# Performance work log

Hardware: AMD Instinct MI355X
Metric: run time of the kernel (lower is better)

## Reference

```python
import jax, jax.numpy as jnp
import numpy as np

L = 16384   # nodes (rows)
E = 131072  # edges
SP = 20000  # column positions (nodes + periodic images)
C = 512     # embed_dim
H = 8       # heads
DH = C // H # head dim = 64
HID = 1024  # ffn hidden


def setup_inputs() -> dict:
    key = jax.random.key(0)
    ks = jax.random.split(key, 16)
    p = lambda k, shape: jax.random.normal(k, shape, dtype=jnp.float32) * 0.02
    return dict(
        x=jax.random.normal(ks[0], (L, C), dtype=jnp.float32),
        row_index=jax.random.randint(ks[1], (E,), 0, L),
        col_index=jax.random.randint(ks[2], (E,), 0, L),
        to_col_index=jax.random.randint(ks[3], (E,), 0, SP),
        att_bias=jax.random.normal(ks[4], (E, H), dtype=jnp.float32),
        pos_att_bias=jax.random.normal(ks[5], (E, H), dtype=jnp.float32),
        dist=jax.random.uniform(ks[6], (E,), minval=0.5, maxval=5.0),
        pos=jax.random.normal(ks[7], (L, 3), dtype=jnp.float32),
        col_pos=jax.random.normal(ks[8], (SP, 3), dtype=jnp.float32),
        ln1_g=jnp.ones((C,), jnp.float32), ln1_b=jnp.zeros((C,), jnp.float32),
        ln2_g=jnp.ones((C,), jnp.float32), ln2_b=jnp.zeros((C,), jnp.float32),
        Wq=p(ks[9], (C, C)), bq=jnp.zeros((C,), jnp.float32),
        Wk=p(ks[10], (C, C)), bk=jnp.zeros((C,), jnp.float32),
        Wv=p(ks[11], (C, C)), bv=jnp.zeros((C,), jnp.float32),
        Wvec=p(ks[12], (3, C)), bvec=jnp.zeros((C,), jnp.float32),
        Wo=p(ks[13], (C, C)), bo=jnp.zeros((C,), jnp.float32),
        W1=p(ks[14], (C, HID)), b1=jnp.zeros((HID,), jnp.float32),
        W2=p(ks[15], (HID, C)), b2=jnp.zeros((C,), jnp.float32),
    )


def _ln(x, g, b, eps=1e-5):
    mu = jnp.mean(x, -1, keepdims=True)
    v = jnp.mean((x - mu) ** 2, -1, keepdims=True)
    return (x - mu) * jax.lax.rsqrt(v + eps) * g + b


def reference(x, row_index, col_index, to_col_index, att_bias, pos_att_bias,
              dist, pos, col_pos, ln1_g, ln1_b, ln2_g, ln2_b,
              Wq, bq, Wk, bk, Wv, bv, Wvec, bvec, Wo, bo, W1, b1, W2, b2):
    Lx = x.shape[0]
    # --- pre-norm + Euclidean sparse attention ---
    z = _ln(x, ln1_g, ln1_b)
    q = (z @ Wq + bq).reshape(Lx, H, DH)
    k = (z @ Wk + bk).reshape(Lx, H, DH)
    v = (z @ Wv + bv).reshape(Lx, H, DH)
    qe = q[row_index]          # (E,H,DH) gather
    ke = k[col_index]          # (E,H,DH)
    ve = v[col_index]          # (E,H,DH)
    # relative unit direction from receiving node to (PBC-shifted) column node
    rel = (col_pos[to_col_index] - pos[row_index]) / dist[:, None]   # (E,3)
    ve = ve + (rel @ Wvec + bvec).reshape(-1, H, DH)
    # Euclidean (negative squared L2) attention score + positional bias
    score = -jnp.sum((qe - ke) ** 2, axis=-1) / np.float32(np.sqrt(DH)) + pos_att_bias  # (E,H)
    # segment softmax over edges grouped by row_index
    m = jax.ops.segment_max(score, row_index, num_segments=Lx)       # (L,H)
    m = jnp.where(jnp.isfinite(m), m, 0.0)
    pexp = jnp.exp(score - m[row_index])
    den = jax.ops.segment_sum(pexp, row_index, num_segments=Lx)      # (L,H)
    deng = den[row_index]
    alpha = pexp / jnp.where(deng == 0.0, 1.0, deng)                 # (E,H)
    out = jax.ops.segment_sum(alpha[:, :, None] * ve, row_index, num_segments=Lx)
    att = out.reshape(Lx, C) @ Wo + bo
    x = x + att
    # --- pre-norm + feed-forward ---
    z2 = _ln(x, ln2_g, ln2_b)
    ff = jax.nn.gelu(z2 @ W1 + b1) @ W2 + b2
    return x + ff
```

## Files before the change

kernel.cpp:

```cpp
#include <hip/hip_runtime.h>

#define L_NODES 16384
#define E_EDGES 131072
#define CDIM 512
#define QKVDIM 1536
#define HEADS 8
#define DHEAD 64
#define HID 1024

typedef __attribute__((ext_vector_type(8))) short bf16x8;
typedef __attribute__((ext_vector_type(4))) float f32x4;

__device__ inline unsigned short f2b(float f) {
    union { float f; unsigned int u; } v{f};
    unsigned int r = (v.u + 0x7fffu + ((v.u >> 16) & 1u)) >> 16;
    return (unsigned short)r;
}
__device__ inline float b2f(unsigned short h) {
    union { unsigned int u; float f; } v;
    v.u = (unsigned int)h << 16;
    return v.f;
}

__device__ inline void async_lds16(const void* g, void* l) {
    __builtin_amdgcn_global_load_lds(
        (const __attribute__((address_space(1))) unsigned int*)g,
        (__attribute__((address_space(3))) unsigned int*)l,
        16, 0, 0);
}

__global__ __launch_bounds__(256) void ln_bf16_kernel(
    const float* __restrict__ x, const float* __restrict__ g,
    const float* __restrict__ b, short* __restrict__ out)
{
    int row = blockIdx.x;
    int t = threadIdx.x;
    const float2* xr = (const float2*)(x + (size_t)row * CDIM);
    float2 v = xr[t];
    float s = v.x + v.y;
    float sq = v.x * v.x + v.y * v.y;
    for (int off = 32; off; off >>= 1) {
        s += __shfl_xor(s, off);
        sq += __shfl_xor(sq, off);
    }
    __shared__ float ss[4], sqs[4];
    int wave = t >> 6, lane = t & 63;
    if (lane == 0) { ss[wave] = s; sqs[wave] = sq; }
    __syncthreads();
    s = ss[0] + ss[1] + ss[2] + ss[3];
    sq = sqs[0] + sqs[1] + sqs[2] + sqs[3];
    float mu = s * (1.0f / CDIM);
    float var = sq * (1.0f / CDIM) - mu * mu;
    float inv = rsqrtf(var + 1e-5f);
    int c = t * 2;
    unsigned short h0 = f2b((v.x - mu) * inv * g[c] + b[c]);
    unsigned short h1 = f2b((v.y - mu) * inv * g[c + 1] + b[c + 1]);
    unsigned int packed = ((unsigned int)h1 << 16) | h0;
    *(unsigned int*)(out + (size_t)row * CDIM + c) = packed;
}

__global__ __launch_bounds__(256) void prep_kernel(
    const float* __restrict__ Wq, const float* __restrict__ Wk,
    const float* __restrict__ Wv, const float* __restrict__ Wo,
    const float* __restrict__ W1, const float* __restrict__ W2,
    short* __restrict__ wqkvT, short* __restrict__ woT,
    short* __restrict__ w1T, short* __restrict__ w2T,
    const float* __restrict__ bq, const float* __restrict__ bk,
    const float* __restrict__ bv, float* __restrict__ bqkv,
    int* __restrict__ cnt)
{
    int bid = blockIdx.x;
    if (bid >= 2054) {
        cnt[(bid - 2054) * 256 + threadIdx.x] = 0;
        return;
    }
    if (bid >= 2048) {
        int i = (bid - 2048) * 256 + threadIdx.x;
        float val = (i < CDIM) ? bq[i] : (i < 2 * CDIM) ? bk[i - CDIM] : bv[i - 2 * CDIM];
        bqkv[i] = val;
        return;
    }
    const float* W; short* WT; int K, N, tn, tk;
    if (bid < 1024) {
        int w = bid >> 8, local = bid & 255;
        tn = local & 15; tk = local >> 4; K = 512; N = 512;
        W = (w == 0) ? Wq : (w == 1) ? Wk : (w == 2) ? Wv : Wo;
        WT = (w == 3) ? woT : wqkvT + (size_t)w * 512 * 512;
    } else if (bid < 1536) {
        int local = bid - 1024;
        tn = local & 31; tk = local >> 5; K = 512; N = 1024;
        W = W1; WT = w1T;
    } else {
        int local = bid - 1536;
        tn = local & 15; tk = local >> 4; K = 1024; N = 512;
        W = W2; WT = w2T;
    }
    __shared__ float tile[32][33];
    int tx = threadIdx.x & 31, ty = threadIdx.x >> 5;
    int n0 = tn * 32, k0 = tk * 32;
#pragma unroll
    for (int r = 0; r < 4; r++)
        tile[ty + r * 8][tx] = W[(size_t)(k0 + ty + r * 8) * N + n0 + tx];
    __syncthreads();
#pragma unroll
    for (int r = 0; r < 4; r++)
        WT[(size_t)(n0 + ty + r * 8) * K + k0 + tx] = f2b(tile[tx][ty + r * 8]);
}

template<int BM>
__global__ __launch_bounds__(256) void gemm_bf16_kernel(
    const short* __restrict__ A, const short* __restrict__ B,
    const float* __restrict__ bias, const float* __restrict__ res,
    float* __restrict__ outf, short* __restrict__ outb,
    int M, int N, int K, int act)
{
    constexpr int MI = BM / 32;
    constexpr int LPI_A = BM / 64;
    constexpr int STAGE_A = BM * 64;
    constexpr int STAGE_B = 8192;
    __shared__ short As[3 * BM * 32];
    __shared__ short Bs[3 * 128 * 32];
    int t = threadIdx.x;
    int bm = blockIdx.y * BM, bn = blockIdx.x * 128;
    int wave = t >> 6, lane = t & 63;
    int wm = (wave & 1) * (BM / 2), wn = (wave >> 1) * 64;
    int crow = lane & 15, quad = lane >> 4;

    f32x4 acc[MI][4] = {};

    const int niter = K >> 5;
    auto stage = [&](int s, int k0) {
#pragma unroll
        for (int a = 0; a < LPI_A; a++) {
            int idx = a * 256 + t;
            int row = idx >> 2, chunk = idx & 3;
            async_lds16(A + (size_t)(bm + row) * K + k0 + chunk * 8,
                        (char*)As + s * STAGE_A + idx * 16);
        }
#pragma unroll
        for (int c = 0; c < 2; c++) {
            int idx = c * 256 + t;
            int row = idx >> 2, chunk = idx & 3;
            async_lds16(B + (size_t)(bn + row) * K + k0 + chunk * 8,
                        (char*)Bs + s * STAGE_B + idx * 16);
        }
    };

    stage(0, 0);
    stage(1, 32);

    for (int i = 0; i < niter; ++i) {
        int cur = i % 3;
        if (i + 1 < niter) {
            if constexpr (BM == 256)      asm volatile("s_waitcnt vmcnt(6)" ::: "memory");
            else if constexpr (BM == 128) asm volatile("s_waitcnt vmcnt(4)" ::: "memory");
            else                          asm volatile("s_waitcnt vmcnt(3)" ::: "memory");
        } else {
            asm volatile("s_waitcnt vmcnt(0)" ::: "memory");
        }
        __builtin_amdgcn_s_barrier();
        if (i + 2 < niter) stage((i + 2) % 3, (i + 2) << 5);

        const short* Ab = As + cur * (BM * 32);
        const short* Bb = Bs + cur * (128 * 32);
        bf16x8 af[MI], bg[4];
#pragma unroll
        for (int ii = 0; ii < MI; ii++)
            af[ii] = *(const bf16x8*)&Ab[(wm + ii * 16 + crow) * 32 + quad * 8];
#pragma unroll
        for (int j = 0; j < 4; j++)
            bg[j] = *(const bf16x8*)&Bb[(wn + j * 16 + crow) * 32 + quad * 8];
#pragma unroll
        for (int ii = 0; ii < MI; ii++)
#pragma unroll
            for (int j = 0; j < 4; j++)
                acc[ii][j] = __builtin_amdgcn_mfma_f32_16x16x32_bf16(af[ii], bg[j], acc[ii][j], 0, 0, 0);
    }

#pragma unroll
    for (int i = 0; i < MI; i++) {
#pragma unroll
        for (int j = 0; j < 4; j++) {
            int n = bn + wn + j * 16 + crow;
            float bi = bias ? bias[n] : 0.0f;
#pragma unroll
            for (int r = 0; r < 4; r++) {
                int mrow = bm + wm + i * 16 + quad * 4 + r;
                float val = acc[i][j][r] + bi;
                if (act) {
                    float u = 1.5957691216057308f * (val + 0.044715f * val * val * val);
                    val = val / (1.0f + __expf(-u));
                }
                if (res) val += res[(size_t)mrow * N + n];
                if (outf) outf[(size_t)mrow * N + n] = val;
                if (outb) outb[(size_t)mrow * N + n] = f2b(val);
            }
        }
    }
}

__global__ void hist_kernel(const int* __restrict__ row_index, int* __restrict__ cnt)
{
    int e = blockIdx.x * 256 + threadIdx.x;
    if (e < E_EDGES) atomicAdd(&cnt[row_index[e]], 1);
}

__global__ __launch_bounds__(1024) void scan_kernel(
    const int* __restrict__ cnt, int* __restrict__ row_start,
    int* __restrict__ cursor)
{
    int t = threadIdx.x;
    int4 c0 = ((const int4*)cnt)[t * 4 + 0];
    int4 c1 = ((const int4*)cnt)[t * 4 + 1];
    int4 c2 = ((const int4*)cnt)[t * 4 + 2];
    int4 c3 = ((const int4*)cnt)[t * 4 + 3];
    int v[16] = {c0.x, c0.y, c0.z, c0.w, c1.x, c1.y, c1.z, c1.w,
                 c2.x, c2.y, c2.z, c2.w, c3.x, c3.y, c3.z, c3.w};
    int total = 0;
    int pfx[16];
#pragma unroll
    for (int i = 0; i < 16; i++) { pfx[i] = total; total += v[i]; }
    int lane = t & 63, wv = t >> 6;
    int incl = total;
    for (int off = 1; off < 64; off <<= 1) {
        int u = __shfl_up(incl, off);
        if (lane >= off) incl += u;
    }
    __shared__ int wsum[16];
    if (lane == 63) wsum[wv] = incl;
    __syncthreads();
    __shared__ int wbase[16];
    if (t < 16) {
        int s = wsum[t];
        int run = 0;
        for (int i = 0; i < 16; i++) { if (i < t) run += wsum[i]; }
        wbase[t] = run;
        (void)s;
    }
    __syncthreads();
    int base = wbase[wv] + (incl - total);
#pragma unroll
    for (int i = 0; i < 4; i++) {
        int4 rs = make_int4(base + pfx[i * 4], base + pfx[i * 4 + 1],
                            base + pfx[i * 4 + 2], base + pfx[i * 4 + 3]);
        ((int4*)row_start)[t * 4 + i] = rs;
        ((int4*)cursor)[t * 4 + i] = rs;
    }
    if (t == 1023) row_start[L_NODES] = base + total;
}

__global__ void scatter_kernel(const int* __restrict__ row_index, const int* __restrict__ col_index,
                               const int* __restrict__ to_col_index, const float* __restrict__ dist,
                               const float* __restrict__ pos, const float* __restrict__ col_pos,
                               const float* __restrict__ pos_att_bias,
                               int* __restrict__ cursor, int4* __restrict__ emeta,
                               float* __restrict__ pabp)
{
    int e = blockIdx.x * 256 + threadIdx.x;
    if (e < E_EDGES) {
        int row = row_index[e];
        int p = atomicAdd(&cursor[row], 1);
        int tci = to_col_index[e];
        float dinv = 1.0f / dist[e];
        float r0 = (col_pos[tci * 3]     - pos[row * 3])     * dinv;
        float r1 = (col_pos[tci * 3 + 1] - pos[row * 3 + 1]) * dinv;
        float r2 = (col_pos[tci * 3 + 2] - pos[row * 3 + 2]) * dinv;
        emeta[p] = make_int4(col_index[e], __float_as_int(r0), __float_as_int(r1),
                             __float_as_int(r2));
        const float4* pb = (const float4*)(pos_att_bias + (size_t)e * HEADS);
        float4 b0 = pb[0], b1 = pb[1];
        float4* dst = (float4*)(pabp + (size_t)p * HEADS);
        dst[0] = b0; dst[1] = b1;
    }
}

__global__ __launch_bounds__(256) void attn_kernel(
    const short* __restrict__ qkv, const int4* __restrict__ emeta,
    const float* __restrict__ pabp, const int* __restrict__ row_start,
    const float* __restrict__ Wvec, const float* __restrict__ bvec,
    short* __restrict__ out_bf)
{
    int lane = threadIdx.x & 63;
    int r = blockIdx.x * 4 + (threadIdx.x >> 6);
    int h = lane >> 3;
    int cbase = lane * 8;

    float qv[8], wv0[8], wv1[8], wv2[8], bvv[8];
    {
        bf16x8 qh = *(const bf16x8*)(qkv + (size_t)r * QKVDIM + cbase);
#pragma unroll
        for (int j = 0; j < 8; j++) qv[j] = b2f((unsigned short)qh[j]);
        float4 a0 = *(const float4*)(Wvec + cbase);
        float4 a1 = *(const float4*)(Wvec + cbase + 4);
        float4 b0 = *(const float4*)(Wvec + CDIM + cbase);
        float4 b1 = *(const float4*)(Wvec + CDIM + cbase + 4);
        float4 c0 = *(const float4*)(Wvec + 2 * CDIM + cbase);
        float4 c1 = *(const float4*)(Wvec + 2 * CDIM + cbase + 4);
        float4 d0 = *(const float4*)(bvec + cbase);
        float4 d1 = *(const float4*)(bvec + cbase + 4);
        wv0[0]=a0.x; wv0[1]=a0.y; wv0[2]=a0.z; wv0[3]=a0.w; wv0[4]=a1.x; wv0[5]=a1.y; wv0[6]=a1.z; wv0[7]=a1.w;
        wv1[0]=b0.x; wv1[1]=b0.y; wv1[2]=b0.z; wv1[3]=b0.w; wv1[4]=b1.x; wv1[5]=b1.y; wv1[6]=b1.z; wv1[7]=b1.w;
        wv2[0]=c0.x; wv2[1]=c0.y; wv2[2]=c0.z; wv2[3]=c0.w; wv2[4]=c1.x; wv2[5]=c1.y; wv2[6]=c1.z; wv2[7]=c1.w;
        bvv[0]=d0.x; bvv[1]=d0.y; bvv[2]=d0.z; bvv[3]=d0.w; bvv[4]=d1.x; bvv[5]=d1.y; bvv[6]=d1.z; bvv[7]=d1.w;
    }

    int e0 = row_start[r], e1 = row_start[r + 1];
    float m = -1e30f, l = 0.0f;
    float acc[8] = {};

    int4 em_n, em_n2;
    float pab_n;
    bf16x8 k_n, v_n;
    if (e0 < e1) {
        em_n = emeta[e0];
        em_n2 = emeta[(e0 + 1 < e1) ? e0 + 1 : e1 - 1];
        pab_n = pabp[(size_t)e0 * HEADS + h];
        const short* kp = qkv + (size_t)em_n.x * QKVDIM + CDIM + cbase;
        k_n = *(const bf16x8*)kp;
        v_n = *(const bf16x8*)(kp + CDIM);
    }
    for (int idx = e0; idx < e1; ++idx) {
        int4 em = em_n;
        float pab = pab_n;
        bf16x8 k8 = k_n, v8 = v_n;
        em_n = em_n2;
        int i2 = (idx + 2 < e1) ? idx + 2 : e1 - 1;
        em_n2 = emeta[i2];
        int i1 = (idx + 1 < e1) ? idx + 1 : e1 - 1;
        pab_n = pabp[(size_t)i1 * HEADS + h];
        {
            const short* kp = qkv + (size_t)em_n.x * QKVDIM + CDIM + cbase;
            k_n = *(const bf16x8*)kp;
            v_n = *(const bf16x8*)(kp + CDIM);
        }
        float s = 0.0f;
        float vf[8];
#pragma unroll
        for (int j = 0; j < 8; j++) {
            float kf = b2f((unsigned short)k8[j]);
            vf[j] = b2f((unsigned short)v8[j]);
            float d = qv[j] - kf;
            s = fmaf(d, d, s);
        }
        s += __shfl_xor(s, 1);
        s += __shfl_xor(s, 2);
        s += __shfl_xor(s, 4);
        float score = -s * 0.125f + pab;
        float mn = fmaxf(m, score);
        float scale = __expf(m - mn);
        float pexp = __expf(score - mn);
        m = mn;
        l = l * scale + pexp;
        float r0 = __int_as_float(em.y), r1 = __int_as_float(em.z), r2 = __int_as_float(em.w);
#pragma unroll
        for (int j = 0; j < 8; j++) {
            float vv = vf[j] + r0 * wv0[j] + r1 * wv1[j] + r2 * wv2[j] + bvv[j];
            acc[j] = fmaf(acc[j], scale, pexp * vv);
        }
    }
    float inv = (l > 0.0f) ? 1.0f / l : 0.0f;
    bf16x8 o;
#pragma unroll
    for (int j = 0; j < 8; j++) o[j] = (short)f2b(acc[j] * inv);
    *(bf16x8*)(out_bf + (size_t)r * CDIM + cbase) = o;
}

extern "C" void kernel_launch(void* const* d_in, const int* in_sizes, int n_in,
                              void* d_out, int out_size, void* d_ws, size_t ws_size,
                              hipStream_t stream)
{
    const float* x            = (const float*)d_in[0];
    const int*   row_index    = (const int*)d_in[1];
    const int*   col_index    = (const int*)d_in[2];
    const int*   to_col_index = (const int*)d_in[3];
    const float* pos_att_bias = (const float*)d_in[5];
    const float* dist         = (const float*)d_in[6];
    const float* pos          = (const float*)d_in[7];
    const float* col_pos      = (const float*)d_in[8];
    const float* ln1_g = (const float*)d_in[9];
    const float* ln1_b = (const float*)d_in[10];
    const float* ln2_g = (const float*)d_in[11];
    const float* ln2_b = (const float*)d_in[12];
    const float* Wq = (const float*)d_in[13];  const float* bq = (const float*)d_in[14];
    const float* Wk = (const float*)d_in[15];  const float* bk = (const float*)d_in[16];
    const float* Wv = (const float*)d_in[17];  const float* bv = (const float*)d_in[18];
    const float* Wvec = (const float*)d_in[19]; const float* bvec = (const float*)d_in[20];
    const float* Wo = (const float*)d_in[21];  const float* bo = (const float*)d_in[22];
    const float* W1 = (const float*)d_in[23];  const float* b1 = (const float*)d_in[24];
    const float* W2 = (const float*)d_in[25];  const float* b2 = (const float*)d_in[26];

    char* ws = (char*)d_ws;
    size_t off = 0;
    auto alloc = [&](size_t bytes) -> void* {
        void* p = ws + off;
        off = (off + bytes + 255) & ~(size_t)255;
        return p;
    };
    const size_t LC = (size_t)L_NODES * CDIM;
    short* qkvb = (short*)alloc((size_t)L_NODES * QKVDIM * 2);
    float* x1f  = (float*)alloc(LC * 4);
    short* zbf  = (short*)alloc(LC * 2);
    short* abf  = (short*)alloc(LC * 2);
    short* wqkvT = (short*)alloc((size_t)QKVDIM * CDIM * 2);
    short* woT   = (short*)alloc((size_t)CDIM * CDIM * 2);
    short* w1T   = (short*)alloc((size_t)CDIM * HID * 2);
    short* w2T   = (short*)alloc((size_t)HID * CDIM * 2);
    float* bqkv  = (float*)alloc(QKVDIM * 4);
    int* cnt       = (int*)alloc(L_NODES * 4);
    int* cursor    = (int*)alloc(L_NODES * 4);
    int* row_start = (int*)alloc((L_NODES + 1) * 4);
    int4* emeta    = (int4*)alloc((size_t)E_EDGES * 16);
    short* hbf = (short*)qkvb;
    float* pabp = x1f;

    prep_kernel<<<2118, 256, 0, stream>>>(Wq, Wk, Wv, Wo, W1, W2,
                                          wqkvT, woT, w1T, w2T,
                                          bq, bk, bv, bqkv, cnt);

    ln_bf16_kernel<<<L_NODES, 256, 0, stream>>>(x, ln1_g, ln1_b, zbf);

    dim3 gqkv(QKVDIM / 128, L_NODES / 256);
    gemm_bf16_kernel<256><<<gqkv, 256, 0, stream>>>(zbf, wqkvT, bqkv, nullptr, nullptr, qkvb,
                                                    L_NODES, QKVDIM, CDIM, 0);

    hist_kernel<<<E_EDGES / 256, 256, 0, stream>>>(row_index, cnt);
    scan_kernel<<<1, 1024, 0, stream>>>(cnt, row_start, cursor);
    scatter_kernel<<<E_EDGES / 256, 256, 0, stream>>>(row_index, col_index, to_col_index,
                                                      dist, pos, col_pos, pos_att_bias,
                                                      cursor, emeta, pabp);

    attn_kernel<<<L_NODES / 4, 256, 0, stream>>>(qkvb, emeta, pabp, row_start, Wvec, bvec, abf);

    dim3 gwo(CDIM / 128, L_NODES / 64);
    gemm_bf16_kernel<64><<<gwo, 256, 0, stream>>>(abf, woT, bo, x, x1f, nullptr, L_NODES, CDIM, CDIM, 0);

    ln_bf16_kernel<<<L_NODES, 256, 0, stream>>>(x1f, ln2_g, ln2_b, zbf);

    dim3 g1024(HID / 128, L_NODES / 256);
    gemm_bf16_kernel<256><<<g1024, 256, 0, stream>>>(zbf, w1T, b1, nullptr, nullptr, hbf, L_NODES, HID, CDIM, 1);
    dim3 gw2(CDIM / 128, L_NODES / 64);
    gemm_bf16_kernel<64><<<gw2, 256, 0, stream>>>(hbf, w2T, b2, x1f, (float*)d_out, nullptr, L_NODES, CDIM, HID, 0);
}
```

Before: 467.1 us.

## Add wave-private double-buffered GEMM for QKV and FFN1 projections

Adds a GEMM kernel in which each of the four waves stages its own 64x32 A and B tiles into a private LDS region with double buffering. This removes block-wide barriers; each wave waits only on its own vmcnt and lgkmcnt. The QKV and W1 GEMMs now use 128x128 block tiles in place of 256x128, while the BM=64 shared-tile kernel is kept for the Wo and W2 GEMMs. In exchange, A and B tiles are no longer shared across waves, so global and L2 traffic per FLOP roughly doubles.

```diff
diff --git a/kernel.cpp b/kernel.cpp
--- a/kernel.cpp
+++ b/kernel.cpp
@@ -27,6 +27,13 @@
         (const __attribute__((address_space(1))) unsigned int*)g,
         (__attribute__((address_space(3))) unsigned int*)l,
         16, 0, 0);
+}
+
+__device__ inline void gelu_res_store(float& val, int act) {
+    if (act) {
+        float u = 1.5957691216057308f * (val + 0.044715f * val * val * val);
+        val = val / (1.0f + __expf(-u));
+    }
 }
 
 __global__ __launch_bounds__(256) void ln_bf16_kernel(
@@ -107,42 +114,112 @@
         WT[(size_t)(n0 + ty + r * 8) * K + k0 + tx] = f2b(tile[tx][ty + r * 8]);
 }
 
-template<int BM>
+__global__ __launch_bounds__(256) void gemm_wp_kernel(
+    const short* __restrict__ A, const short* __restrict__ B,
+    const float* __restrict__ bias, const float* __restrict__ res,
+    float* __restrict__ outf, short* __restrict__ outb,
+    int M, int N, int K, int act)
+{
+    __shared__ short lds[4 * 2 * 4096];
+    int t = threadIdx.x;
+    int wave = t >> 6, lane = t & 63;
+    int bm = blockIdx.y * 128 + (wave & 1) * 64;
+    int bn = blockIdx.x * 128 + (wave >> 1) * 64;
+    int crow = lane & 15, quad = lane >> 4;
+    short* wbase = lds + wave * 8192;
+
+    f32x4 acc[4][4] = {};
+    const int niter = K >> 5;
+
+    auto stage = [&](int s, int k0) {
+        short* dstA = wbase + s * 4096;
+        short* dstB = dstA + 2048;
+        int row = (lane >> 2), chunk = lane & 3;
+#pragma unroll
+        for (int a = 0; a < 4; a++)
+            async_lds16(A + (size_t)(bm + a * 16 + row) * K + k0 + chunk * 8,
+                        (char*)dstA + a * 1024 + lane * 16);
+#pragma unroll
+        for (int a = 0; a < 4; a++)
+            async_lds16(B + (size_t)(bn + a * 16 + row) * K + k0 + chunk * 8,
+                        (char*)dstB + a * 1024 + lane * 16);
+    };
+
+    stage(0, 0);
+    stage(1, 32);
+
+    for (int i = 0; i < niter; ++i) {
+        const short* Ab = wbase + (i & 1) * 4096;
+        const short* Bb = Ab + 2048;
+        if (i + 1 < niter) asm volatile("s_waitcnt vmcnt(8)" ::: "memory");
+        else               asm volatile("s_waitcnt vmcnt(0)" ::: "memory");
+        bf16x8 af[4], bg[4];
+#pragma unroll
+        for (int ii = 0; ii < 4; ii++)
+            af[ii] = *(const bf16x8*)&Ab[(ii * 16 + crow) * 32 + quad * 8];
+#pragma unroll
+        for (int j = 0; j < 4; j++)
+            bg[j] = *(const bf16x8*)&Bb[(j * 16 + crow) * 32 + quad * 8];
+        asm volatile("s_waitcnt lgkmcnt(0)" ::: "memory");
+        if (i + 2 < niter) stage(i & 1, (i + 2) << 5);
+#pragma unroll
+        for (int ii = 0; ii < 4; ii++)
+#pragma unroll
+            for (int j = 0; j < 4; j++)
+                acc[ii][j] = __builtin_amdgcn_mfma_f32_16x16x32_bf16(af[ii], bg[j], acc[ii][j], 0, 0, 0);
+    }
+
+#pragma unroll
+    for (int i = 0; i < 4; i++) {
+#pragma unroll
+        for (int j = 0; j < 4; j++) {
+            int n = bn + j * 16 + crow;
+            float bi = bias ? bias[n] : 0.0f;
+#pragma unroll
+            for (int r = 0; r < 4; r++) {
+                int mrow = bm + i * 16 + quad * 4 + r;
+                float val = acc[i][j][r] + bi;
+                gelu_res_store(val, act);
+                if (res) val += res[(size_t)mrow * N + n];
+                if (outf) outf[(size_t)mrow * N + n] = val;
+                if (outb) outb[(size_t)mrow * N + n] = f2b(val);
+            }
+        }
+    }
+}
+
 __global__ __launch_bounds__(256) void gemm_bf16_kernel(
     const short* __restrict__ A, const short* __restrict__ B,
     const float* __restrict__ bias, const float* __restrict__ res,
     float* __restrict__ outf, short* __restrict__ outb,
     int M, int N, int K, int act)
 {
-    constexpr int MI = BM / 32;
-    constexpr int LPI_A = BM / 64;
-    constexpr int STAGE_A = BM * 64;
-    constexpr int STAGE_B = 8192;
+    constexpr int BM = 64;
+    constexpr int MI = 2;
     __shared__ short As[3 * BM * 32];
     __shared__ short Bs[3 * 128 * 32];
     int t = threadIdx.x;
     int bm = blockIdx.y * BM, bn = blockIdx.x * 128;
     int wave = t >> 6, lane = t & 63;
-    int wm = (wave & 1) * (BM / 2), wn = (wave >> 1) * 64;
+    int wm = (wave & 1) * 32, wn = (wave >> 1) * 64;
     int crow = lane & 15, quad = lane >> 4;
 
     f32x4 acc[MI][4] = {};
 
     const int niter = K >> 5;
     auto stage = [&](int s, int k0) {
-#pragma unroll
-        for (int a = 0; a < LPI_A; a++) {
-            int idx = a * 256 + t;
+        {
+            int idx = t;
             int row = idx >> 2, chunk = idx & 3;
             async_lds16(A + (size_t)(bm + row) * K + k0 + chunk * 8,
-                        (char*)As + s * STAGE_A + idx * 16);
+                        (char*)As + s * 4096 + idx * 16);
         }
 #pragma unroll
         for (int c = 0; c < 2; c++) {
             int idx = c * 256 + t;
             int row = idx >> 2, chunk = idx & 3;
             async_lds16(B + (size_t)(bn + row) * K + k0 + chunk * 8,
-                        (char*)Bs + s * STAGE_B + idx * 16);
+                        (char*)Bs + s * 8192 + idx * 16);
         }
     };
 
@@ -151,13 +228,8 @@
 
     for (int i = 0; i < niter; ++i) {
         int cur = i % 3;
-        if (i + 1 < niter) {
-            if constexpr (BM == 256)      asm volatile("s_waitcnt vmcnt(6)" ::: "memory");
-            else if constexpr (BM == 128) asm volatile("s_waitcnt vmcnt(4)" ::: "memory");
-            else                          asm volatile("s_waitcnt vmcnt(3)" ::: "memory");
-        } else {
-            asm volatile("s_waitcnt vmcnt(0)" ::: "memory");
-        }
+        if (i + 1 < niter) asm volatile("s_waitcnt vmcnt(3)" ::: "memory");
+        else               asm volatile("s_waitcnt vmcnt(0)" ::: "memory");
         __builtin_amdgcn_s_barrier();
         if (i + 2 < niter) stage((i + 2) % 3, (i + 2) << 5);
 
@@ -187,10 +259,7 @@
             for (int r = 0; r < 4; r++) {
                 int mrow = bm + wm + i * 16 + quad * 4 + r;
                 float val = acc[i][j][r] + bi;
-                if (act) {
-                    float u = 1.5957691216057308f * (val + 0.044715f * val * val * val);
-                    val = val / (1.0f + __expf(-u));
-                }
+                gelu_res_store(val, act);
                 if (res) val += res[(size_t)mrow * N + n];
                 if (outf) outf[(size_t)mrow * N + n] = val;
                 if (outb) outb[(size_t)mrow * N + n] = f2b(val);
@@ -231,11 +300,9 @@
     __syncthreads();
     __shared__ int wbase[16];
     if (t < 16) {
-        int s = wsum[t];
         int run = 0;
         for (int i = 0; i < 16; i++) { if (i < t) run += wsum[i]; }
         wbase[t] = run;
-        (void)s;
     }
     __syncthreads();
     int base = wbase[wv] + (incl - total);
@@ -419,9 +486,9 @@
 
     ln_bf16_kernel<<<L_NODES, 256, 0, stream>>>(x, ln1_g, ln1_b, zbf);
 
-    dim3 gqkv(QKVDIM / 128, L_NODES / 256);
-    gemm_bf16_kernel<256><<<gqkv, 256, 0, stream>>>(zbf, wqkvT, bqkv, nullptr, nullptr, qkvb,
-                                                    L_NODES, QKVDIM, CDIM, 0);
+    dim3 gqkv(QKVDIM / 128, L_NODES / 128);
+    gemm_wp_kernel<<<gqkv, 256, 0, stream>>>(zbf, wqkvT, bqkv, nullptr, nullptr, qkvb,
+                                             L_NODES, QKVDIM, CDIM, 0);
 
     hist_kernel<<<E_EDGES / 256, 256, 0, stream>>>(row_index, cnt);
     scan_kernel<<<1, 1024, 0, stream>>>(cnt, row_start, cursor);
@@ -432,12 +499,12 @@
     attn_kernel<<<L_NODES / 4, 256, 0, stream>>>(qkvb, emeta, pabp, row_start, Wvec, bvec, abf);
 
     dim3 gwo(CDIM / 128, L_NODES / 64);
-    gemm_bf16_kernel<64><<<gwo, 256, 0, stream>>>(abf, woT, bo, x, x1f, nullptr, L_NODES, CDIM, CDIM, 0);
+    gemm_bf16_kernel<<<gwo, 256, 0, stream>>>(abf, woT, bo, x, x1f, nullptr, L_NODES, CDIM, CDIM, 0);
 
     ln_bf16_kernel<<<L_NODES, 256, 0, stream>>>(x1f, ln2_g, ln2_b, zbf);
 
-    dim3 g1024(HID / 128, L_NODES / 256);
-    gemm_bf16_kernel<256><<<g1024, 256, 0, stream>>>(zbf, w1T, b1, nullptr, nullptr, hbf, L_NODES, HID, CDIM, 1);
+    dim3 g1024(HID / 128, L_NODES / 128);
+    gemm_wp_kernel<<<g1024, 256, 0, stream>>>(zbf, w1T, b1, nullptr, nullptr, hbf, L_NODES, HID, CDIM, 1);
     dim3 gw2(CDIM / 128, L_NODES / 64);
-    gemm_bf16_kernel<64><<<gw2, 256, 0, stream>>>(hbf, w2T, b2, x1f, (float*)d_out, nullptr, L_NODES, CDIM, HID, 0);
-}
+    gemm_bf16_kernel<<<gw2, 256, 0, stream>>>(hbf, w2T, b2, x1f, (float*)d_out, nullptr, L_NODES, CDIM, HID, 0);
+}
```

After: 411.4 us. 1.14x faster.
